# Optimization experiments

Measured on AMD Instinct MI355X. Metric: run time of the kernel, lower is better.

The kernel has to match this reference:

```python
import jax, jax.numpy as jnp
import numpy as np

N, E, F_IN, H, C = 100000, 1600000, 128, 128, 40

def setup_inputs() -> dict:
    key = jax.random.key(0)
    ks = jax.random.split(key, 8)
    s = 0.05  # param init scale
    return {
        "x": jax.random.normal(ks[0], (N, F_IN), dtype=jnp.float32),
        "edge_index": jax.random.randint(ks[1], (2, E), 0, N, dtype=jnp.int64),
        "W1_rel": jax.random.normal(ks[2], (H, F_IN), dtype=jnp.float32) * s,
        "b1": jnp.zeros((H,), dtype=jnp.float32),
        "W1_root": jax.random.normal(ks[3], (H, F_IN), dtype=jnp.float32) * s,
        "W2_rel": jax.random.normal(ks[4], (C, H), dtype=jnp.float32) * s,
        "b2": jnp.zeros((C,), dtype=jnp.float32),
        "W2_root": jax.random.normal(ks[5], (C, H), dtype=jnp.float32) * s,
    }

def _graph_conv(x, src, dst, W_rel, b, W_root, n_nodes):
    # PyG GraphConv: lin_rel(sum_{j in N(i)} x_j) + lin_root(x_i); lin_root has no bias
    agg = jax.ops.segment_sum(x[src], dst, num_segments=n_nodes)  # [N, F]
    return agg @ W_rel.T + b + x @ W_root.T

def reference(x, edge_index, W1_rel, b1, W1_root, W2_rel, b2, W2_root):
    src, dst = edge_index[0], edge_index[1]
    h = _graph_conv(x, src, dst, W1_rel, b1, W1_root, N)
    h = jax.nn.relu(h)  # dropout is identity in eval mode
    out = _graph_conv(h, src, dst, W2_rel, b2, W2_root, N)
    return jax.nn.log_softmax(out, axis=1)
```

## Files before the change

### kernel.cpp

```cpp
#include <hip/hip_runtime.h>
#include <hip/hip_bf16.h>
#include <math.h>

typedef __bf16 bf16x8 __attribute__((ext_vector_type(8)));
typedef float f32x4 __attribute__((ext_vector_type(4)));
typedef float f32x2 __attribute__((ext_vector_type(2)));
typedef unsigned int uint32;

#define CHUNK 8192
#define MAXBINS 512

__device__ __forceinline__ float bflo(uint32 u) { return __uint_as_float(u << 16); }
__device__ __forceinline__ float bfhi(uint32 u) { return __uint_as_float(u & 0xffff0000u); }
__device__ __forceinline__ unsigned short tobf(float f) {
    return __builtin_bit_cast(unsigned short, __float2bfloat16(f));
}
__device__ __forceinline__ unsigned char tofp8(float f) {
    return (unsigned char)(__builtin_amdgcn_cvt_pk_fp8_f32(f, f, 0, false) & 0xff);
}


__global__ __launch_bounds__(256) void binhist_kernel(
    const int* __restrict__ dst, int* __restrict__ blkhist,
    int nE, int nChunks, int nBins)
{
    __shared__ int h[MAXBINS];
    int blk = blockIdx.x, t = threadIdx.x;
    for (int i = t; i < nBins; i += 256) h[i] = 0;
    __syncthreads();
    int e0 = blk * CHUNK;
    int e1 = e0 + CHUNK; if (e1 > nE) e1 = nE;
    for (int e = e0 + t; e < e1; e += 256)
        atomicAdd(&h[dst[e] >> 8], 1);
    __syncthreads();
    for (int b = t; b < nBins; b += 256)
        blkhist[(size_t)b * nChunks + blk] = h[b];
}

__global__ __launch_bounds__(256) void csr_partial_kernel(
    const int* __restrict__ cnt, int* __restrict__ blocksum, int nN)
{
    int b = blockIdx.x, t = threadIdx.x;
    int base = b * 1024 + t * 4;
    int s = 0;
    #pragma unroll
    for (int k = 0; k < 4; ++k) { int i = base + k; if (i < nN) s += cnt[i]; }
    #pragma unroll
    for (int off = 1; off < 64; off <<= 1) s += __shfl_xor(s, off);
    __shared__ int ws[4];
    int lane = t & 63, w = t >> 6;
    if (lane == 0) ws[w] = s;
    __syncthreads();
    if (t == 0) blocksum[b] = ws[0] + ws[1] + ws[2] + ws[3];
}

__global__ __launch_bounds__(1024) void csr_scanblocks_kernel(
    const int* __restrict__ blocksum, int* __restrict__ blockpre,
    int nB, int* __restrict__ outtot, int nN)
{
    __shared__ int sm[1024];
    int t = threadIdx.x;
    int v = (t < nB) ? blocksum[t] : 0;
    sm[t] = v;
    __syncthreads();
    for (int off = 1; off < 1024; off <<= 1) {
        int u = (t >= off) ? sm[t - off] : 0;
        __syncthreads();
        sm[t] += u;
        __syncthreads();
    }
    if (t < nB) blockpre[t] = sm[t] - v;
    if (t == 1023) outtot[nN] = sm[1023];
}

__global__ __launch_bounds__(256) void csr_scanfinal_kernel(
    const int* __restrict__ cnt, const int* __restrict__ blockpre,
    int* __restrict__ out, int nN)
{
    int b = blockIdx.x, t = threadIdx.x;
    int base = b * 1024 + t * 4;
    int c[4]; int s = 0;
    #pragma unroll
    for (int k = 0; k < 4; ++k) { int i = base + k; c[k] = (i < nN) ? cnt[i] : 0; s += c[k]; }
    int lane = t & 63, w = t >> 6;
    int inc = s;
    #pragma unroll
    for (int off = 1; off < 64; off <<= 1) {
        int u = __shfl_up(inc, off);
        if (lane >= off) inc += u;
    }
    __shared__ int ws[4];
    if (lane == 63) ws[w] = inc;
    __syncthreads();
    int wpre = 0;
    for (int i = 0; i < w; ++i) wpre += ws[i];
    int run = blockpre[b] + wpre + (inc - s);
    #pragma unroll
    for (int k = 0; k < 4; ++k) {
        int i = base + k;
        if (i < nN) { out[i] = run; run += c[k]; }
    }
}

__global__ __launch_bounds__(256) void binscatter_kernel(
    const int* __restrict__ src, const int* __restrict__ dst,
    const int* __restrict__ blkbase, uint32* __restrict__ packed,
    int nE, int nChunks, int nBins)
{
    __shared__ int h[MAXBINS];
    int blk = blockIdx.x, t = threadIdx.x;
    for (int i = t; i < nBins; i += 256) h[i] = 0;
    __syncthreads();
    int e0 = blk * CHUNK;
    int e1 = e0 + CHUNK; if (e1 > nE) e1 = nE;
    for (int e = e0 + t; e < e1; e += 256) {
        int d = dst[e];
        int b = d >> 8;
        int r = atomicAdd(&h[b], 1);
        int pos = blkbase[(size_t)b * nChunks + blk] + r;
        packed[pos] = (uint32)src[e] | ((uint32)(d & 255) << 24);
    }
}

__global__ __launch_bounds__(256) void binsort_kernel(
    const uint32* __restrict__ packed, const int* __restrict__ blkbase,
    int* __restrict__ rowptr, int* __restrict__ sorted_src,
    int nChunks, int nBins, int nN, int nE)
{
    __shared__ int h[256];
    __shared__ int offs[256];
    __shared__ int ws[4];
    int b = blockIdx.x, t = threadIdx.x;
    int segbase = blkbase[(size_t)b * nChunks];
    int segend  = (b + 1 < nBins) ? blkbase[(size_t)(b + 1) * nChunks] : nE;

    h[t] = 0;
    __syncthreads();
    for (int i = segbase + t; i < segend; i += 256)
        atomicAdd(&h[packed[i] >> 24], 1);
    __syncthreads();

    int c = h[t];
    int lane = t & 63, w = t >> 6;
    int inc = c;
    #pragma unroll
    for (int off = 1; off < 64; off <<= 1) {
        int u = __shfl_up(inc, off);
        if (lane >= off) inc += u;
    }
    if (lane == 63) ws[w] = inc;
    __syncthreads();
    int wpre = 0;
    for (int i = 0; i < w; ++i) wpre += ws[i];
    int ex = wpre + inc - c;
    offs[t] = ex;
    int node = b * 256 + t;
    if (node < nN) rowptr[node] = segbase + ex;
    if (b == 0 && t == 0) rowptr[nN] = nE;
    __syncthreads();

    for (int i = segbase + t; i < segend; i += 256) {
        uint32 pk = packed[i];
        int ld = (int)(pk >> 24);
        int r = atomicAdd(&offs[ld], 1);
        sorted_src[segbase + r] = (int)(pk & 0x00FFFFFFu);
    }
}


__global__ __launch_bounds__(256) void cvt_fp8_kernel(
    const float4* __restrict__ in, uint32* __restrict__ out, int n4)
{
    int i = blockIdx.x * blockDim.x + threadIdx.x;
    int stride = gridDim.x * blockDim.x;
    for (; i < n4; i += stride) {
        float4 v = in[i];
        int w = __builtin_amdgcn_cvt_pk_fp8_f32(v.x, v.y, 0, false);
        w = __builtin_amdgcn_cvt_pk_fp8_f32(v.z, v.w, w, true);
        out[i] = (uint32)w;
    }
}

__global__ __launch_bounds__(256) void prep_weights_kernel(
    const float* __restrict__ W1_rel, const float* __restrict__ W1_root,
    const float* __restrict__ W2_rel, const float* __restrict__ W2_root,
    unsigned short* __restrict__ W1relB, unsigned short* __restrict__ W1rootB,
    unsigned short* __restrict__ Wpq)
{
    int i = blockIdx.x * 256 + threadIdx.x;
    if (i < 16384) {
        W1relB[i] = tobf(W1_rel[i]);
    } else if (i < 32768) {
        int j = i - 16384;
        W1rootB[j] = tobf(W1_root[j]);
    } else if (i < 49152) {
        int j = i - 32768;
        int o = j >> 7, k = j & 127;
        float v = 0.f;
        if (o < 40) v = W2_rel[o * 128 + k];
        else if (o >= 64 && o < 104) v = W2_root[(o - 64) * 128 + k];
        Wpq[j] = tobf(v);
    }
}

__global__ __launch_bounds__(256) void aggregate_fp8_kernel(
    const uint32* __restrict__ xf8u,
    const int* __restrict__ rowptr,
    const int* __restrict__ sorted_src,
    uint2* __restrict__ aggout2,
    int nN)
{
    int wave = threadIdx.x >> 6;
    int lane = threadIdx.x & 63;
    int node = blockIdx.x * 4 + wave;
    if (node >= nN) return;
    int half = lane >> 5, l32 = lane & 31;
    int beg = rowptr[node], end = rowptr[node + 1];
    float a0 = 0.f, a1 = 0.f, a2 = 0.f, a3 = 0.f;
    int j = beg;
    for (; j + 8 <= end; j += 8) {
        uint32 u0 = xf8u[(size_t)sorted_src[j + half] * 32 + l32];
        uint32 u1 = xf8u[(size_t)sorted_src[j + 2 + half] * 32 + l32];
        uint32 u2 = xf8u[(size_t)sorted_src[j + 4 + half] * 32 + l32];
        uint32 u3 = xf8u[(size_t)sorted_src[j + 6 + half] * 32 + l32];
        f32x2 p0 = __builtin_amdgcn_cvt_pk_f32_fp8(u0, false);
        f32x2 q0 = __builtin_amdgcn_cvt_pk_f32_fp8(u0, true);
        f32x2 p1 = __builtin_amdgcn_cvt_pk_f32_fp8(u1, false);
        f32x2 q1 = __builtin_amdgcn_cvt_pk_f32_fp8(u1, true);
        f32x2 p2 = __builtin_amdgcn_cvt_pk_f32_fp8(u2, false);
        f32x2 q2 = __builtin_amdgcn_cvt_pk_f32_fp8(u2, true);
        f32x2 p3 = __builtin_amdgcn_cvt_pk_f32_fp8(u3, false);
        f32x2 q3 = __builtin_amdgcn_cvt_pk_f32_fp8(u3, true);
        a0 += (p0[0] + p1[0]) + (p2[0] + p3[0]);
        a1 += (p0[1] + p1[1]) + (p2[1] + p3[1]);
        a2 += (q0[0] + q1[0]) + (q2[0] + q3[0]);
        a3 += (q0[1] + q1[1]) + (q2[1] + q3[1]);
    }
    for (; j + 2 <= end; j += 2) {
        uint32 u = xf8u[(size_t)sorted_src[j + half] * 32 + l32];
        f32x2 p0 = __builtin_amdgcn_cvt_pk_f32_fp8(u, false);
        f32x2 p1 = __builtin_amdgcn_cvt_pk_f32_fp8(u, true);
        a0 += p0[0]; a1 += p0[1]; a2 += p1[0]; a3 += p1[1];
    }
    if (j < end && half == 0) {
        uint32 u = xf8u[(size_t)sorted_src[j] * 32 + l32];
        f32x2 p0 = __builtin_amdgcn_cvt_pk_f32_fp8(u, false);
        f32x2 p1 = __builtin_amdgcn_cvt_pk_f32_fp8(u, true);
        a0 += p0[0]; a1 += p0[1]; a2 += p1[0]; a3 += p1[1];
    }
    a0 += __shfl_xor(a0, 32);
    a1 += __shfl_xor(a1, 32);
    a2 += __shfl_xor(a2, 32);
    a3 += __shfl_xor(a3, 32);
    if (half == 0) {
        uint2 o;
        o.x = (uint32)tobf(a0) | ((uint32)tobf(a1) << 16);
        o.y = (uint32)tobf(a2) | ((uint32)tobf(a3) << 16);
        aggout2[(size_t)node * 32 + l32] = o;
    }
}

__global__ __launch_bounds__(256) void gemm1_kernel(
    const unsigned short* __restrict__ aggb,
    const float* __restrict__ xf,
    const unsigned short* __restrict__ Wrel,
    const unsigned short* __restrict__ Wroot,
    const float* __restrict__ b1,
    unsigned short* __restrict__ hb,
    int nN)
{
    __shared__ __align__(16) unsigned char lds[32768];
    int tid = threadIdx.x;
    int wave = tid >> 6, lane = tid & 63;
    int i0 = blockIdx.x * 64 + wave * 16;
    int mrow = lane & 15, kslot = lane >> 4;
    int arow = i0 + mrow; if (arow >= nN) arow = 0;

    f32x4 acc[8] = {};
    const unsigned short* Wsrc[2] = {Wrel, Wroot};

    for (int ph = 0; ph < 2; ++ph) {
        __syncthreads();
        const uint4* src = (const uint4*)Wsrc[ph];
        for (int c = tid; c < 2048; c += 256) {
            int row = c >> 4;
            int off = (c & 15) << 4;
            *(uint4*)(&lds[row * 256 + (off ^ ((row & 7) << 4))]) = src[c];
        }
        __syncthreads();
        if (ph == 0) {
            const unsigned short* Ap = aggb + (size_t)arow * 128 + kslot * 8;
            #pragma unroll
            for (int t = 0; t < 4; ++t) {
                bf16x8 a = *(const bf16x8*)(Ap + t * 32);
                #pragma unroll
                for (int ct = 0; ct < 8; ++ct) {
                    int o = ct * 16 + mrow;
                    int off = (t * 64 + kslot * 16) ^ ((o & 7) << 4);
                    bf16x8 b = *(const bf16x8*)(&lds[o * 256 + off]);
                    acc[ct] = __builtin_amdgcn_mfma_f32_16x16x32_bf16(a, b, acc[ct], 0, 0, 0);
                }
            }
        } else {
            const float* Ap = xf + (size_t)arow * 128 + kslot * 8;
            #pragma unroll
            for (int t = 0; t < 4; ++t) {
                float4 f0 = *(const float4*)(Ap + t * 32);
                float4 f1 = *(const float4*)(Ap + t * 32 + 4);
                union { bf16x8 v; unsigned short u[8]; } a;
                a.u[0] = tobf(f0.x); a.u[1] = tobf(f0.y);
                a.u[2] = tobf(f0.z); a.u[3] = tobf(f0.w);
                a.u[4] = tobf(f1.x); a.u[5] = tobf(f1.y);
                a.u[6] = tobf(f1.z); a.u[7] = tobf(f1.w);
                #pragma unroll
                for (int ct = 0; ct < 8; ++ct) {
                    int o = ct * 16 + mrow;
                    int off = (t * 64 + kslot * 16) ^ ((o & 7) << 4);
                    bf16x8 b = *(const bf16x8*)(&lds[o * 256 + off]);
                    acc[ct] = __builtin_amdgcn_mfma_f32_16x16x32_bf16(a.v, b, acc[ct], 0, 0, 0);
                }
            }
        }
    }
    #pragma unroll
    for (int ct = 0; ct < 8; ++ct) {
        int col = ct * 16 + mrow;
        float bias = b1[col];
        #pragma unroll
        for (int r = 0; r < 4; ++r) {
            int row = i0 + kslot * 4 + r;
            if (row < nN)
                hb[(size_t)row * 128 + col] = tobf(fmaxf(acc[ct][r] + bias, 0.f));
        }
    }
}

__global__ __launch_bounds__(256) void gemm_pq_kernel(
    const unsigned short* __restrict__ hb,
    const unsigned short* __restrict__ Wpq,
    unsigned char* __restrict__ pf8,
    unsigned short* __restrict__ qb,
    int nN)
{
    __shared__ __align__(16) unsigned char lds[32768];
    int tid = threadIdx.x;
    int wave = tid >> 6, lane = tid & 63;
    int i0 = blockIdx.x * 64 + wave * 16;
    int mrow = lane & 15, kslot = lane >> 4;
    int arow = i0 + mrow; if (arow >= nN) arow = 0;

    const uint4* src = (const uint4*)Wpq;
    for (int c = tid; c < 2048; c += 256) {
        int row = c >> 4;
        int off = (c & 15) << 4;
        *(uint4*)(&lds[row * 256 + (off ^ ((row & 7) << 4))]) = src[c];
    }
    __syncthreads();

    f32x4 acc[8] = {};
    const unsigned short* Ap = hb + (size_t)arow * 128 + kslot * 8;
    #pragma unroll
    for (int t = 0; t < 4; ++t) {
        bf16x8 a = *(const bf16x8*)(Ap + t * 32);
        #pragma unroll
        for (int ct = 0; ct < 8; ++ct) {
            int o = ct * 16 + mrow;
            int off = (t * 64 + kslot * 16) ^ ((o & 7) << 4);
            bf16x8 b = *(const bf16x8*)(&lds[o * 256 + off]);
            acc[ct] = __builtin_amdgcn_mfma_f32_16x16x32_bf16(a, b, acc[ct], 0, 0, 0);
        }
    }
    #pragma unroll
    for (int ct = 0; ct < 8; ++ct) {
        int col = ct * 16 + mrow;
        #pragma unroll
        for (int r = 0; r < 4; ++r) {
            int row = i0 + kslot * 4 + r;
            if (row < nN) {
                if (col < 64) pf8[(size_t)row * 64 + col] = tofp8(acc[ct][r]);
                else          qb[(size_t)row * 64 + (col - 64)] = tobf(acc[ct][r]);
            }
        }
    }
}

__global__ __launch_bounds__(256) void final_lsm_kernel(
    const unsigned short* __restrict__ pf8u,
    const uint32* __restrict__ qbu,
    const int* __restrict__ rowptr,
    const int* __restrict__ sorted_src,
    const float* __restrict__ b2,
    float* __restrict__ out,
    int nN)
{
    int wave = threadIdx.x >> 6;
    int lane = threadIdx.x & 63;
    int node = blockIdx.x * 4 + wave;
    if (node >= nN) return;
    int half = lane >> 5, l32 = lane & 31;
    int beg = rowptr[node], end = rowptr[node + 1];

    float a0 = 0.f, a1 = 0.f;
    int j = beg;
    for (; j + 8 <= end; j += 8) {
        uint32 u0 = pf8u[(size_t)sorted_src[j + half] * 32 + l32];
        uint32 u1 = pf8u[(size_t)sorted_src[j + 2 + half] * 32 + l32];
        uint32 u2 = pf8u[(size_t)sorted_src[j + 4 + half] * 32 + l32];
        uint32 u3 = pf8u[(size_t)sorted_src[j + 6 + half] * 32 + l32];
        f32x2 p0 = __builtin_amdgcn_cvt_pk_f32_fp8(u0, false);
        f32x2 p1 = __builtin_amdgcn_cvt_pk_f32_fp8(u1, false);
        f32x2 p2 = __builtin_amdgcn_cvt_pk_f32_fp8(u2, false);
        f32x2 p3 = __builtin_amdgcn_cvt_pk_f32_fp8(u3, false);
        a0 += (p0[0] + p1[0]) + (p2[0] + p3[0]);
        a1 += (p0[1] + p1[1]) + (p2[1] + p3[1]);
    }
    for (; j + 2 <= end; j += 2) {
        uint32 u = pf8u[(size_t)sorted_src[j + half] * 32 + l32];
        f32x2 p0 = __builtin_amdgcn_cvt_pk_f32_fp8(u, false);
        a0 += p0[0]; a1 += p0[1];
    }
    if (j < end && half == 0) {
        uint32 u = pf8u[(size_t)sorted_src[j] * 32 + l32];
        f32x2 p0 = __builtin_amdgcn_cvt_pk_f32_fp8(u, false);
        a0 += p0[0]; a1 += p0[1];
    }
    a0 += __shfl_xor(a0, 32);
    a1 += __shfl_xor(a1, 32);

    float v0, v1;
    if (l32 < 20) {
        uint32 uq = qbu[(size_t)node * 32 + l32];
        float2 bb = *(const float2*)(b2 + 2 * l32);
        v0 = a0 + bflo(uq) + bb.x;
        v1 = a1 + bfhi(uq) + bb.y;
    } else {
        v0 = v1 = -INFINITY;
    }

    float m = fmaxf(v0, v1);
    #pragma unroll
    for (int off = 16; off >= 1; off >>= 1) m = fmaxf(m, __shfl_xor(m, off));
    float s = (l32 < 20) ? (expf(v0 - m) + expf(v1 - m)) : 0.f;
    #pragma unroll
    for (int off = 16; off >= 1; off >>= 1) s += __shfl_xor(s, off);
    float lse = m + logf(s);

    if (half == 0 && l32 < 20) {
        float2 o = make_float2(v0 - lse, v1 - lse);
        *(float2*)(out + (size_t)node * 40 + 2 * l32) = o;
    }
}


static inline char* alignup(char* p, size_t a) {
    return (char*)(((uintptr_t)p + a - 1) & ~(uintptr_t)(a - 1));
}

extern "C" void kernel_launch(void* const* d_in, const int* in_sizes, int n_in,
                              void* d_out, int out_size, void* d_ws, size_t ws_size,
                              hipStream_t stream)
{
    const float* x       = (const float*)d_in[0];
    const int*   ei      = (const int*)d_in[1];
    const float* W1_rel  = (const float*)d_in[2];
    const float* b1      = (const float*)d_in[3];
    const float* W1_root = (const float*)d_in[4];
    const float* W2_rel  = (const float*)d_in[5];
    const float* b2      = (const float*)d_in[6];
    const float* W2_root = (const float*)d_in[7];

    int N = in_sizes[0] / 128;
    int E = in_sizes[1] / 2;
    const int* srcp = ei;
    const int* dstp = ei + E;

    int nChunks = (E + CHUNK - 1) / CHUNK;
    int nBins   = (N + 255) >> 8;
    int nScan   = nBins * nChunks;
    int nB2     = (nScan + 1023) / 1024;
    size_t nf = (size_t)N * 128;

    char* p = (char*)d_ws;
    unsigned char*  xf8     = (unsigned char*)p;   p += nf;
    unsigned short* aggb    = (unsigned short*)p;  p += nf * 2;
    unsigned short* hb      = (unsigned short*)p;  p += nf * 2;
    unsigned short* W1relB  = (unsigned short*)p;  p += 16384 * 2;
    unsigned short* W1rootB = (unsigned short*)p;  p += 16384 * 2;
    unsigned short* Wpq     = (unsigned short*)p;  p += 16384 * 2;
    p = alignup(p, 16);
    int* rowptr     = (int*)p;  p += (size_t)(N + 1) * 4;
    p = alignup(p, 16);
    int* blkhist    = (int*)p;  p += (size_t)nScan * 4;
    int* blkbase    = (int*)p;  p += (size_t)(nScan + 1) * 4;
    int* blocksum   = (int*)p;  p += (size_t)nB2 * 4;
    int* blockpre   = (int*)p;  p += (size_t)nB2 * 4;
    p = alignup(p, 16);
    uint32* packed  = (uint32*)p; p += (size_t)E * 4;
    p = alignup(p, 16);
    int* sorted_src = (int*)p;  p += (size_t)E * 4;

    unsigned short* qb  = aggb;
    unsigned char*  pf8 = (unsigned char*)(aggb + (size_t)N * 64);

    if ((size_t)(p - (char*)d_ws) > ws_size || nBins > MAXBINS) return;

    binhist_kernel<<<nChunks, 256, 0, stream>>>(dstp, blkhist, E, nChunks, nBins);
    csr_partial_kernel<<<nB2, 256, 0, stream>>>(blkhist, blocksum, nScan);
    csr_scanblocks_kernel<<<1, 1024, 0, stream>>>(blocksum, blockpre, nB2, blkbase, nScan);
    csr_scanfinal_kernel<<<nB2, 256, 0, stream>>>(blkhist, blockpre, blkbase, nScan);
    binscatter_kernel<<<nChunks, 256, 0, stream>>>(srcp, dstp, blkbase, packed, E, nChunks, nBins);
    binsort_kernel<<<nBins, 256, 0, stream>>>(packed, blkbase, rowptr, sorted_src,
                                              nChunks, nBins, N, E);

    cvt_fp8_kernel<<<2048, 256, 0, stream>>>((const float4*)x, (uint32*)xf8, (int)(nf / 4));
    prep_weights_kernel<<<192, 256, 0, stream>>>(
        W1_rel, W1_root, W2_rel, W2_root, W1relB, W1rootB, Wpq);

    aggregate_fp8_kernel<<<(N + 3) / 4, 256, 0, stream>>>(
        (const uint32*)xf8, rowptr, sorted_src, (uint2*)aggb, N);
    gemm1_kernel<<<(N + 63) / 64, 256, 0, stream>>>(
        aggb, x, W1relB, W1rootB, b1, hb, N);

    gemm_pq_kernel<<<(N + 63) / 64, 256, 0, stream>>>(hb, Wpq, pf8, qb, N);
    final_lsm_kernel<<<(N + 3) / 4, 256, 0, stream>>>(
        (const unsigned short*)pf8, (const uint32*)qb, rowptr, sorted_src,
        b2, (float*)d_out, N);
}
```

Measured before the change: 218.5 us.

## Fuse layer-1 GEMM with layer-2 projection via LDS and pack outputs to 40 columns

Result: faster. 207.4 us (-5.1%).

```diff
diff --git a/kernel.cpp b/kernel.cpp
--- a/kernel.cpp
+++ b/kernel.cpp
@@ -193,12 +193,10 @@
     } else if (i < 32768) {
         int j = i - 16384;
         W1rootB[j] = tobf(W1_root[j]);
-    } else if (i < 49152) {
+    } else if (i < 32768 + 10240) {
         int j = i - 32768;
         int o = j >> 7, k = j & 127;
-        float v = 0.f;
-        if (o < 40) v = W2_rel[o * 128 + k];
-        else if (o >= 64 && o < 104) v = W2_root[(o - 64) * 128 + k];
+        float v = (o < 40) ? W2_rel[o * 128 + k] : W2_root[(o - 40) * 128 + k];
         Wpq[j] = tobf(v);
     }
 }
@@ -260,16 +258,19 @@
     }
 }
 
-__global__ __launch_bounds__(256) void gemm1_kernel(
+__global__ __launch_bounds__(256) void gemm_fused_kernel(
     const unsigned short* __restrict__ aggb,
     const float* __restrict__ xf,
     const unsigned short* __restrict__ Wrel,
     const unsigned short* __restrict__ Wroot,
+    const unsigned short* __restrict__ Wpq,
     const float* __restrict__ b1,
-    unsigned short* __restrict__ hb,
+    unsigned char* __restrict__ pf8,
+    unsigned short* __restrict__ qb,
     int nN)
 {
     __shared__ __align__(16) unsigned char lds[32768];
+    __shared__ __align__(16) unsigned char hlds[16384];
     int tid = threadIdx.x;
     int wave = tid >> 6, lane = tid & 63;
     int i0 = blockIdx.x * 64 + wave * 16;
@@ -322,63 +323,55 @@
             }
         }
     }
+
     #pragma unroll
     for (int ct = 0; ct < 8; ++ct) {
         int col = ct * 16 + mrow;
         float bias = b1[col];
         #pragma unroll
         for (int r = 0; r < 4; ++r) {
-            int row = i0 + kslot * 4 + r;
-            if (row < nN)
-                hb[(size_t)row * 128 + col] = tobf(fmaxf(acc[ct][r] + bias, 0.f));
+            int rl = wave * 16 + kslot * 4 + r;
+            float v = fmaxf(acc[ct][r] + bias, 0.f);
+            *(unsigned short*)(&hlds[rl * 256 + ((col * 2) ^ ((rl & 7) << 4))]) = tobf(v);
         }
     }
-}
-
-__global__ __launch_bounds__(256) void gemm_pq_kernel(
-    const unsigned short* __restrict__ hb,
-    const unsigned short* __restrict__ Wpq,
-    unsigned char* __restrict__ pf8,
-    unsigned short* __restrict__ qb,
-    int nN)
-{
-    __shared__ __align__(16) unsigned char lds[32768];
-    int tid = threadIdx.x;
-    int wave = tid >> 6, lane = tid & 63;
-    int i0 = blockIdx.x * 64 + wave * 16;
-    int mrow = lane & 15, kslot = lane >> 4;
-    int arow = i0 + mrow; if (arow >= nN) arow = 0;
-
-    const uint4* src = (const uint4*)Wpq;
-    for (int c = tid; c < 2048; c += 256) {
-        int row = c >> 4;
-        int off = (c & 15) << 4;
-        *(uint4*)(&lds[row * 256 + (off ^ ((row & 7) << 4))]) = src[c];
-    }
-    __syncthreads();
-
-    f32x4 acc[8] = {};
-    const unsigned short* Ap = hb + (size_t)arow * 128 + kslot * 8;
-    #pragma unroll
-    for (int t = 0; t < 4; ++t) {
-        bf16x8 a = *(const bf16x8*)(Ap + t * 32);
+    __syncthreads();
+
+    {
+        const uint4* src = (const uint4*)Wpq;
+        for (int c = tid; c < 1280; c += 256) {
+            int row = c >> 4;
+            int off = (c & 15) << 4;
+            *(uint4*)(&lds[row * 256 + (off ^ ((row & 7) << 4))]) = src[c];
+        }
+    }
+    __syncthreads();
+
+    f32x4 acc2[5] = {};
+    {
+        int rl = wave * 16 + mrow;
         #pragma unroll
-        for (int ct = 0; ct < 8; ++ct) {
-            int o = ct * 16 + mrow;
-            int off = (t * 64 + kslot * 16) ^ ((o & 7) << 4);
-            bf16x8 b = *(const bf16x8*)(&lds[o * 256 + off]);
-            acc[ct] = __builtin_amdgcn_mfma_f32_16x16x32_bf16(a, b, acc[ct], 0, 0, 0);
+        for (int t = 0; t < 4; ++t) {
+            bf16x8 a = *(const bf16x8*)(&hlds[rl * 256 + ((t * 64 + kslot * 16) ^ ((rl & 7) << 4))]);
+            #pragma unroll
+            for (int ct = 0; ct < 5; ++ct) {
+                int o = ct * 16 + mrow;
+                int off = (t * 64 + kslot * 16) ^ ((o & 7) << 4);
+                bf16x8 b = *(const bf16x8*)(&lds[o * 256 + off]);
+                acc2[ct] = __builtin_amdgcn_mfma_f32_16x16x32_bf16(a, b, acc2[ct], 0, 0, 0);
+            }
         }
     }
-    #pragma unroll
-    for (int ct = 0; ct < 8; ++ct) {
+
+    #pragma unroll
+    for (int ct = 0; ct < 5; ++ct) {
         int col = ct * 16 + mrow;
         #pragma unroll
         for (int r = 0; r < 4; ++r) {
             int row = i0 + kslot * 4 + r;
             if (row < nN) {
-                if (col < 64) pf8[(size_t)row * 64 + col] = tofp8(acc[ct][r]);
-                else          qb[(size_t)row * 64 + (col - 64)] = tobf(acc[ct][r]);
+                if (col < 40) pf8[(size_t)row * 40 + col] = tofp8(acc2[ct][r]);
+                else          qb[(size_t)row * 40 + (col - 40)] = tobf(acc2[ct][r]);
             }
         }
     }
@@ -403,10 +396,10 @@
     float a0 = 0.f, a1 = 0.f;
     int j = beg;
     for (; j + 8 <= end; j += 8) {
-        uint32 u0 = pf8u[(size_t)sorted_src[j + half] * 32 + l32];
-        uint32 u1 = pf8u[(size_t)sorted_src[j + 2 + half] * 32 + l32];
-        uint32 u2 = pf8u[(size_t)sorted_src[j + 4 + half] * 32 + l32];
-        uint32 u3 = pf8u[(size_t)sorted_src[j + 6 + half] * 32 + l32];
+        uint32 u0 = pf8u[(size_t)sorted_src[j + half] * 20 + l32];
+        uint32 u1 = pf8u[(size_t)sorted_src[j + 2 + half] * 20 + l32];
+        uint32 u2 = pf8u[(size_t)sorted_src[j + 4 + half] * 20 + l32];
+        uint32 u3 = pf8u[(size_t)sorted_src[j + 6 + half] * 20 + l32];
         f32x2 p0 = __builtin_amdgcn_cvt_pk_f32_fp8(u0, false);
         f32x2 p1 = __builtin_amdgcn_cvt_pk_f32_fp8(u1, false);
         f32x2 p2 = __builtin_amdgcn_cvt_pk_f32_fp8(u2, false);
@@ -415,12 +408,12 @@
         a1 += (p0[1] + p1[1]) + (p2[1] + p3[1]);
     }
     for (; j + 2 <= end; j += 2) {
-        uint32 u = pf8u[(size_t)sorted_src[j + half] * 32 + l32];
+        uint32 u = pf8u[(size_t)sorted_src[j + half] * 20 + l32];
         f32x2 p0 = __builtin_amdgcn_cvt_pk_f32_fp8(u, false);
         a0 += p0[0]; a1 += p0[1];
     }
     if (j < end && half == 0) {
-        uint32 u = pf8u[(size_t)sorted_src[j] * 32 + l32];
+        uint32 u = pf8u[(size_t)sorted_src[j] * 20 + l32];
         f32x2 p0 = __builtin_amdgcn_cvt_pk_f32_fp8(u, false);
         a0 += p0[0]; a1 += p0[1];
     }
@@ -429,7 +422,7 @@
 
     float v0, v1;
     if (l32 < 20) {
-        uint32 uq = qbu[(size_t)node * 32 + l32];
+        uint32 uq = qbu[(size_t)node * 20 + l32];
         float2 bb = *(const float2*)(b2 + 2 * l32);
         v0 = a0 + bflo(uq) + bb.x;
         v1 = a1 + bfhi(uq) + bb.y;
@@ -483,10 +476,14 @@
     char* p = (char*)d_ws;
     unsigned char*  xf8     = (unsigned char*)p;   p += nf;
     unsigned short* aggb    = (unsigned short*)p;  p += nf * 2;
-    unsigned short* hb      = (unsigned short*)p;  p += nf * 2;
+    p = alignup(p, 16);
+    unsigned short* qb      = (unsigned short*)p;  p += (size_t)N * 40 * 2;
+    p = alignup(p, 16);
+    unsigned char*  pf8     = (unsigned char*)p;   p += (size_t)N * 40 + 64;
+    p = alignup(p, 16);
     unsigned short* W1relB  = (unsigned short*)p;  p += 16384 * 2;
     unsigned short* W1rootB = (unsigned short*)p;  p += 16384 * 2;
-    unsigned short* Wpq     = (unsigned short*)p;  p += 16384 * 2;
+    unsigned short* Wpq     = (unsigned short*)p;  p += 10240 * 2;
     p = alignup(p, 16);
     int* rowptr     = (int*)p;  p += (size_t)(N + 1) * 4;
     p = alignup(p, 16);
@@ -498,9 +495,6 @@
     uint32* packed  = (uint32*)p; p += (size_t)E * 4;
     p = alignup(p, 16);
     int* sorted_src = (int*)p;  p += (size_t)E * 4;
-
-    unsigned short* qb  = aggb;
-    unsigned char*  pf8 = (unsigned char*)(aggb + (size_t)N * 64);
 
     if ((size_t)(p - (char*)d_ws) > ws_size || nBins > MAXBINS) return;
 
@@ -513,15 +507,15 @@
                                               nChunks, nBins, N, E);
 
     cvt_fp8_kernel<<<2048, 256, 0, stream>>>((const float4*)x, (uint32*)xf8, (int)(nf / 4));
-    prep_weights_kernel<<<192, 256, 0, stream>>>(
+    prep_weights_kernel<<<(43008 + 255) / 256, 256, 0, stream>>>(
         W1_rel, W1_root, W2_rel, W2_root, W1relB, W1rootB, Wpq);
 
     aggregate_fp8_kernel<<<(N + 3) / 4, 256, 0, stream>>>(
         (const uint32*)xf8, rowptr, sorted_src, (uint2*)aggb, N);
-    gemm1_kernel<<<(N + 63) / 64, 256, 0, stream>>>(
-        aggb, x, W1relB, W1rootB, b1, hb, N);
-
-    gemm_pq_kernel<<<(N + 63) / 64, 256, 0, stream>>>(hb, Wpq, pf8, qb, N);
+
+    gemm_fused_kernel<<<(N + 63) / 64, 256, 0, stream>>>(
+        aggb, x, W1relB, W1rootB, Wpq, b1, pf8, qb, N);
+
     final_lsm_kernel<<<(N + 3) / 4, 256, 0, stream>>>(
         (const unsigned short*)pf8, (const uint32*)qb, rowptr, sorted_src,
         b2, (float*)d_out, N);
```
